# Kernel optimization log

Measured on AMD Instinct MI355X. Metric: run time of the kernel, lower is better.

Reference implementation:

```python
import jax, jax.numpy as jnp
import numpy as np

B, T, D, H = 32, 1024, 1024, 128


def setup_inputs() -> dict:
    key = jax.random.key(0)
    k = jax.random.split(key, 5)
    s = 1.0 / np.sqrt(H)  # pytorch LSTM init scale
    return {
        "x": jax.random.normal(k[0], (B, T, D), dtype=jnp.float32),
        "W_ih": jax.random.uniform(k[1], (4 * H, D), minval=-s, maxval=s, dtype=jnp.float32),
        "W_hh": jax.random.uniform(k[2], (4 * H, H), minval=-s, maxval=s, dtype=jnp.float32),
        "b_ih": jax.random.uniform(k[3], (4 * H,), minval=-s, maxval=s, dtype=jnp.float32),
        "b_hh": jax.random.uniform(k[4], (4 * H,), minval=-s, maxval=s, dtype=jnp.float32),
    }


def reference(x, W_ih, W_hh, b_ih, b_hh):
    # x: [B, T, D]. Single-layer unidirectional LSTM, batch_first, zero init state.
    # Gate order matches PyTorch: i, f, g, o.
    b, t, d = x.shape
    h = W_hh.shape[1]
    # Fuse the input-side GEMM across all timesteps: [B, T, 4H]
    gx = jnp.einsum('btd,gd->btg', x, W_ih) + b_ih + b_hh

    def step(carry, g_t):
        h_prev, c_prev = carry
        g = g_t + h_prev @ W_hh.T  # [B, 4H]
        i, f, gg, o = jnp.split(g, 4, axis=-1)
        i = jax.nn.sigmoid(i)
        f = jax.nn.sigmoid(f)
        gg = jnp.tanh(gg)
        o = jax.nn.sigmoid(o)
        c = f * c_prev + i * gg
        hn = o * jnp.tanh(c)
        return (hn, c), hn

    h0 = jnp.zeros((b, h), dtype=x.dtype)
    c0 = jnp.zeros((b, h), dtype=x.dtype)
    (h_n, c_n), hs = jax.lax.scan(step, (h0, c0), jnp.swapaxes(gx, 0, 1))
    out = jnp.swapaxes(hs, 0, 1)  # [B, T, H]
    # Mirrors torch: (output, (h_n[1,B,H], c_n[1,B,H]))
    return out, h_n[None], c_n[None]
```

## Files before the change

kernel.cpp:

```cpp
#include <hip/hip_runtime.h>
#include <hip/hip_fp16.h>
#include <cstdint>
#include <cstddef>


typedef __attribute__((ext_vector_type(8))) _Float16 half8;
typedef __attribute__((ext_vector_type(4))) _Float16 half4;
typedef __attribute__((ext_vector_type(4))) float    f32x4;

#define BT    32768
#define DD    1024
#define GG    512
#define HH    128
#define TT    1024
#define BB    32

__global__ void prep_kernel(const float* __restrict__ wih,
                            const float* __restrict__ whh,
                            const float* __restrict__ bih,
                            const float* __restrict__ bhh,
                            _Float16* __restrict__ wih_h,
                            __half*   __restrict__ whh_h,
                            float* __restrict__ bsum) {
    int i = blockIdx.x * 256 + threadIdx.x;
    wih_h[i] = (_Float16)wih[i];
    if (i < GG * HH) whh_h[i] = __float2half(whh[i]);
    if (i < GG)      bsum[i] = bih[i] + bhh[i];
}

#define BM 128
#define BN 128
#define BK 32
#define LDP 40

__global__ __launch_bounds__(256)
void gemm_gx(const float* __restrict__ x, const _Float16* __restrict__ wih_h,
             const float* __restrict__ bsum, float* __restrict__ gx) {
    const int bid = blockIdx.x;
    const int m0 = (bid >> 2) * BM;
    const int n0 = (bid & 3) * BN;
    const int t  = threadIdx.x;
    const int lane = t & 63;
    const int w  = t >> 6;
    const int wr = w >> 1, wc = w & 1;
    const int lr = lane & 15;
    const int lk = lane >> 4;

    __shared__ __align__(16) _Float16 As[BM][LDP];
    __shared__ __align__(16) _Float16 Bs[BN][LDP];

    f32x4 acc[4][4] = {};

    for (int kt = 0; kt < DD; kt += BK) {
        #pragma unroll
        for (int pass = 0; pass < 4; ++pass) {
            int r = pass * 32 + (t >> 3);
            int c = (t & 7) * 4;
            float4 v = *(const float4*)(x + (size_t)(m0 + r) * DD + kt + c);
            half4 hv;
            hv[0] = (_Float16)v.x; hv[1] = (_Float16)v.y;
            hv[2] = (_Float16)v.z; hv[3] = (_Float16)v.w;
            *(half4*)&As[r][c] = hv;
        }
        #pragma unroll
        for (int pass = 0; pass < 2; ++pass) {
            int r = pass * 64 + (t >> 2);
            int c = (t & 3) * 8;
            float4 v = *(const float4*)(wih_h + (size_t)(n0 + r) * DD + kt + c);
            *(float4*)&Bs[r][c] = v;
        }
        __syncthreads();

        half8 af[4], bf[4];
        #pragma unroll
        for (int i = 0; i < 4; ++i)
            af[i] = *(const half8*)&As[wr * 64 + i * 16 + lr][lk * 8];
        #pragma unroll
        for (int j = 0; j < 4; ++j)
            bf[j] = *(const half8*)&Bs[wc * 64 + j * 16 + lr][lk * 8];

        #pragma unroll
        for (int i = 0; i < 4; ++i)
            #pragma unroll
            for (int j = 0; j < 4; ++j)
                acc[i][j] = __builtin_amdgcn_mfma_f32_16x16x32_f16(af[i], bf[j], acc[i][j], 0, 0, 0);
        __syncthreads();
    }

    #pragma unroll
    for (int j = 0; j < 4; ++j) {
        int n = n0 + wc * 64 + j * 16 + lr;
        float bn = bsum[n];
        #pragma unroll
        for (int i = 0; i < 4; ++i) {
            int mbase = m0 + wr * 64 + i * 16 + lk * 4;
            #pragma unroll
            for (int r = 0; r < 4; ++r)
                gx[(size_t)(mbase + r) * GG + n] = acc[i][j][r] + bn;
        }
    }
}


__device__ __forceinline__ __half2 u2h(uint32_t v) { return *(__half2*)&v; }

template <int CTRL>
__device__ __forceinline__ float dpp_qp(float x) {
    int i = __float_as_int(x);
    i = __builtin_amdgcn_update_dpp(0, i, CTRL, 0xF, 0xF, true);
    return __int_as_float(i);
}
#define QP_XOR1 0xB1
#define QP_XOR2 0x4E

#define LOG2E   1.4426950408889634f

#define WDECL(Q)  uint32_t w##Q##x, w##Q##y, w##Q##z, w##Q##w;
#define WLOAD(Q)  { uint4 u_ = wp[Q]; w##Q##x = u_.x; w##Q##y = u_.y; \
                    w##Q##z = u_.z; w##Q##w = u_.w; }
#define WPIN(Q)   asm volatile("" : "+v"(w##Q##x), "+v"(w##Q##y), \
                                    "+v"(w##Q##z), "+v"(w##Q##w));
#define DOTE(Q)   { uint4 hv_ = hp[Q]; \
    a0 = __hfma2(u2h(w##Q##x), u2h(hv_.x), a0); \
    a1 = __hfma2(u2h(w##Q##y), u2h(hv_.y), a1); \
    a2 = __hfma2(u2h(w##Q##z), u2h(hv_.z), a2); \
    a3 = __hfma2(u2h(w##Q##w), u2h(hv_.w), a3); }
#define DOTO(Q)   { uint4 hv_ = hp[Q]; \
    a4 = __hfma2(u2h(w##Q##x), u2h(hv_.x), a4); \
    a5 = __hfma2(u2h(w##Q##y), u2h(hv_.y), a5); \
    a6 = __hfma2(u2h(w##Q##z), u2h(hv_.z), a6); \
    a7 = __hfma2(u2h(w##Q##w), u2h(hv_.w), a7); }
#define W16(F) F(0) F(1) F(2) F(3) F(4) F(5) F(6) F(7) \
               F(8) F(9) F(10) F(11) F(12) F(13) F(14) F(15)

__global__ __launch_bounds__(512)
__attribute__((amdgpu_waves_per_eu(2, 2)))
void lstm_rec(const float* __restrict__ gx, const __half* __restrict__ whh_h,
              float* __restrict__ out, float* __restrict__ hn, float* __restrict__ cn) {
    const int b  = blockIdx.x;
    const int t  = threadIdx.x;
    const int j  = t >> 2;
    const int gi = t & 3;
    const int r  = gi * HH + j;

    __shared__ __align__(16) __half hbuf[2][HH];
    __shared__ __align__(16) float  oring[64][HH];

    const uint4* wp = (const uint4*)(whh_h + (size_t)r * HH);
    W16(WDECL)
    W16(WLOAD)
    W16(WPIN)

    const float kneg = (gi == 2) ? -2.f * LOG2E : -LOG2E;
    const float k2   = (gi == 2) ?  2.f : 1.f;
    const float k3   = (gi == 2) ? -1.f : 0.f;

    if (t < HH) hbuf[0][t] = __float2half(0.f);
    __syncthreads();

    const float* gxp  = gx + (size_t)b * TT * GG + r;
    float*       outp = out + (size_t)b * TT * HH;

    float c = 0.f, hval = 0.f;
    float p0 = gxp[0];
    float p1 = gxp[GG];

    for (int step = 0; step < TT; ++step) {
        int sp = step + 2; if (sp > TT - 1) sp = TT - 1;
        float p2 = gxp[(size_t)sp * GG];

        const uint4* hp = (const uint4*)hbuf[step & 1];
        __half2 a0, a1, a2, a3, a4, a5, a6, a7;
        a0 = a1 = a2 = a3 = a4 = a5 = a6 = a7 = __float2half2_rn(0.f);
        DOTE(0)  DOTO(1)  DOTE(2)  DOTO(3)
        DOTE(4)  DOTO(5)  DOTE(6)  DOTO(7)
        DOTE(8)  DOTO(9)  DOTE(10) DOTO(11)
        DOTE(12) DOTO(13) DOTE(14) DOTO(15)
        a0 = __hadd2(a0, a4); a1 = __hadd2(a1, a5);
        a2 = __hadd2(a2, a6); a3 = __hadd2(a3, a7);
        a0 = __hadd2(a0, a2); a1 = __hadd2(a1, a3);
        a0 = __hadd2(a0, a1);
        float pre = p0 + __low2float(a0) + __high2float(a0);

        float s = __builtin_amdgcn_rcpf(1.f + __builtin_amdgcn_exp2f(pre * kneg));
        float a = fmaf(k2, s, k3);

        float x1 = dpp_qp<QP_XOR1>(a);
        float x2 = dpp_qp<QP_XOR2>(a);
        float x3 = dpp_qp<QP_XOR2>(x1);

        if (gi == 0) {
            c = fmaf(x1, c, a * x2);
            float th = fmaf(2.f, __builtin_amdgcn_rcpf(
                          1.f + __builtin_amdgcn_exp2f(-2.f * LOG2E * c)), -1.f);
            hval = x3 * th;
            hbuf[(step + 1) & 1][j] = __float2half(hval);
            oring[step & 63][j] = hval;
        }

        __builtin_amdgcn_sched_barrier(0);
        asm volatile("s_waitcnt lgkmcnt(0)" ::: "memory");
        __builtin_amdgcn_s_barrier();
        __builtin_amdgcn_sched_barrier(0);

        if ((step & 63) == 63) {
            float4*       dst = (float4*)(outp + (size_t)(step - 63) * HH);
            const float4* src = (const float4*)&oring[0][0];
            #pragma unroll
            for (int k = 0; k < 4; ++k)
                dst[t + k * 512] = src[t + k * 512];
            __syncthreads();
        }

        p0 = p1; p1 = p2;
    }

    if (gi == 0) {
        hn[b * HH + j] = hval;
        cn[b * HH + j] = c;
    }
}

extern "C" void kernel_launch(void* const* d_in, const int* in_sizes, int n_in,
                              void* d_out, int out_size, void* d_ws, size_t ws_size,
                              hipStream_t stream) {
    const float* x   = (const float*)d_in[0];
    const float* wih = (const float*)d_in[1];
    const float* whh = (const float*)d_in[2];
    const float* bih = (const float*)d_in[3];
    const float* bhh = (const float*)d_in[4];
    float* out = (float*)d_out;

    char* ws = (char*)d_ws;
    _Float16* wih_h = (_Float16*)ws;
    __half*   whh_h = (__half*)(ws + (size_t)(1 << 20));
    float*    bsum  = (float*)(ws + (size_t)(1 << 20) + (128 << 10));
    float*    gx    = (float*)(ws + (size_t)(1 << 20) + (128 << 10) + 4096);

    prep_kernel<<<(GG * DD) / 256, 256, 0, stream>>>(wih, whh, bih, bhh, wih_h, whh_h, bsum);
    gemm_gx<<<(BT / BM) * (GG / BN), 256, 0, stream>>>(x, wih_h, bsum, gx);

    float* hn = out + (size_t)BB * TT * HH;
    float* cn = hn + BB * HH;
    lstm_rec<<<BB, 512, 0, stream>>>(gx, whh_h, out, hn, cn);
}
```

Measured before the change: 804.1 us.

## Split recurrent dot products along K across quad lanes instead of by gate

Each quad of threads now handles one hidden unit. Each lane covers a quarter of the K dimension for all four gates, and the partial sums are reduced with DPP quad shuffles. Each thread reads only 64 bytes of h from LDS per step instead of 256, which cuts LDS traffic on the serial critical path. In exchange, every lane redundantly evaluates all four gate activations and the cell update, and each lane makes four short FMA chains instead of one long one.

Result: no change. 810.2 us (+0.8%).

```diff
diff --git a/kernel.cpp b/kernel.cpp
--- a/kernel.cpp
+++ b/kernel.cpp
@@ -101,7 +101,6 @@
     }
 }
 
-
 __device__ __forceinline__ __half2 u2h(uint32_t v) { return *(__half2*)&v; }
 
 template <int CTRL>
@@ -115,23 +114,35 @@
 
 #define LOG2E   1.4426950408889634f
 
-#define WDECL(Q)  uint32_t w##Q##x, w##Q##y, w##Q##z, w##Q##w;
-#define WLOAD(Q)  { uint4 u_ = wp[Q]; w##Q##x = u_.x; w##Q##y = u_.y; \
-                    w##Q##z = u_.z; w##Q##w = u_.w; }
-#define WPIN(Q)   asm volatile("" : "+v"(w##Q##x), "+v"(w##Q##y), \
-                                    "+v"(w##Q##z), "+v"(w##Q##w));
-#define DOTE(Q)   { uint4 hv_ = hp[Q]; \
-    a0 = __hfma2(u2h(w##Q##x), u2h(hv_.x), a0); \
-    a1 = __hfma2(u2h(w##Q##y), u2h(hv_.y), a1); \
-    a2 = __hfma2(u2h(w##Q##z), u2h(hv_.z), a2); \
-    a3 = __hfma2(u2h(w##Q##w), u2h(hv_.w), a3); }
-#define DOTO(Q)   { uint4 hv_ = hp[Q]; \
-    a4 = __hfma2(u2h(w##Q##x), u2h(hv_.x), a4); \
-    a5 = __hfma2(u2h(w##Q##y), u2h(hv_.y), a5); \
-    a6 = __hfma2(u2h(w##Q##z), u2h(hv_.z), a6); \
-    a7 = __hfma2(u2h(w##Q##w), u2h(hv_.w), a7); }
-#define W16(F) F(0) F(1) F(2) F(3) F(4) F(5) F(6) F(7) \
-               F(8) F(9) F(10) F(11) F(12) F(13) F(14) F(15)
+#define WDECL(G,Q)  uint32_t w##G##Q##x, w##G##Q##y, w##G##Q##z, w##G##Q##w;
+#define WLOAD(G,Q)  { uint4 u_ = wq[((G) * HH + j) * 16 + 4 * s_ + (Q)]; \
+                      w##G##Q##x = u_.x; w##G##Q##y = u_.y; \
+                      w##G##Q##z = u_.z; w##G##Q##w = u_.w; }
+#define WPIN(G,Q)   asm volatile("" : "+v"(w##G##Q##x), "+v"(w##G##Q##y), \
+                                      "+v"(w##G##Q##z), "+v"(w##G##Q##w));
+#define WALL(F) F(0,0) F(0,1) F(0,2) F(0,3)  F(1,0) F(1,1) F(1,2) F(1,3) \
+                F(2,0) F(2,1) F(2,2) F(2,3)  F(3,0) F(3,1) F(3,2) F(3,3)
+
+#define GATE_DOT(G) {                                          \
+    __half2 cA_ = __float2half2_rn(0.f), cB_ = cA_;            \
+    cA_ = __hfma2(u2h(w##G##0x), u2h(h0.x), cA_);              \
+    cA_ = __hfma2(u2h(w##G##0y), u2h(h0.y), cA_);              \
+    cA_ = __hfma2(u2h(w##G##0z), u2h(h0.z), cA_);              \
+    cA_ = __hfma2(u2h(w##G##0w), u2h(h0.w), cA_);              \
+    cA_ = __hfma2(u2h(w##G##1x), u2h(h1.x), cA_);              \
+    cA_ = __hfma2(u2h(w##G##1y), u2h(h1.y), cA_);              \
+    cA_ = __hfma2(u2h(w##G##1z), u2h(h1.z), cA_);              \
+    cA_ = __hfma2(u2h(w##G##1w), u2h(h1.w), cA_);              \
+    cB_ = __hfma2(u2h(w##G##2x), u2h(h2.x), cB_);              \
+    cB_ = __hfma2(u2h(w##G##2y), u2h(h2.y), cB_);              \
+    cB_ = __hfma2(u2h(w##G##2z), u2h(h2.z), cB_);              \
+    cB_ = __hfma2(u2h(w##G##2w), u2h(h2.w), cB_);              \
+    cB_ = __hfma2(u2h(w##G##3x), u2h(h3.x), cB_);              \
+    cB_ = __hfma2(u2h(w##G##3y), u2h(h3.y), cB_);              \
+    cB_ = __hfma2(u2h(w##G##3z), u2h(h3.z), cB_);              \
+    cB_ = __hfma2(u2h(w##G##3w), u2h(h3.w), cB_);              \
+    __half2 t_ = __hadd2(cA_, cB_);                            \
+    P##G = fmaf(msk##G, p0, __low2float(t_) + __high2float(t_)); }
 
 __global__ __launch_bounds__(512)
 __attribute__((amdgpu_waves_per_eu(2, 2)))
@@ -140,25 +151,25 @@
     const int b  = blockIdx.x;
     const int t  = threadIdx.x;
     const int j  = t >> 2;
-    const int gi = t & 3;
-    const int r  = gi * HH + j;
+    const int s_ = t & 3;
 
     __shared__ __align__(16) __half hbuf[2][HH];
     __shared__ __align__(16) float  oring[64][HH];
 
-    const uint4* wp = (const uint4*)(whh_h + (size_t)r * HH);
-    W16(WDECL)
-    W16(WLOAD)
-    W16(WPIN)
-
-    const float kneg = (gi == 2) ? -2.f * LOG2E : -LOG2E;
-    const float k2   = (gi == 2) ?  2.f : 1.f;
-    const float k3   = (gi == 2) ? -1.f : 0.f;
+    const uint4* wq = (const uint4*)whh_h;
+    WALL(WDECL)
+    WALL(WLOAD)
+    WALL(WPIN)
+
+    const float msk0 = (s_ == 0) ? 1.f : 0.f;
+    const float msk1 = (s_ == 1) ? 1.f : 0.f;
+    const float msk2 = (s_ == 2) ? 1.f : 0.f;
+    const float msk3 = (s_ == 3) ? 1.f : 0.f;
 
     if (t < HH) hbuf[0][t] = __float2half(0.f);
     __syncthreads();
 
-    const float* gxp  = gx + (size_t)b * TT * GG + r;
+    const float* gxp  = gx + (size_t)b * TT * GG + (s_ * HH + j);
     float*       outp = out + (size_t)b * TT * HH;
 
     float c = 0.f, hval = 0.f;
@@ -169,31 +180,30 @@
         int sp = step + 2; if (sp > TT - 1) sp = TT - 1;
         float p2 = gxp[(size_t)sp * GG];
 
-        const uint4* hp = (const uint4*)hbuf[step & 1];
-        __half2 a0, a1, a2, a3, a4, a5, a6, a7;
-        a0 = a1 = a2 = a3 = a4 = a5 = a6 = a7 = __float2half2_rn(0.f);
-        DOTE(0)  DOTO(1)  DOTE(2)  DOTO(3)
-        DOTE(4)  DOTO(5)  DOTE(6)  DOTO(7)
-        DOTE(8)  DOTO(9)  DOTE(10) DOTO(11)
-        DOTE(12) DOTO(13) DOTE(14) DOTO(15)
-        a0 = __hadd2(a0, a4); a1 = __hadd2(a1, a5);
-        a2 = __hadd2(a2, a6); a3 = __hadd2(a3, a7);
-        a0 = __hadd2(a0, a2); a1 = __hadd2(a1, a3);
-        a0 = __hadd2(a0, a1);
-        float pre = p0 + __low2float(a0) + __high2float(a0);
-
-        float s = __builtin_amdgcn_rcpf(1.f + __builtin_amdgcn_exp2f(pre * kneg));
-        float a = fmaf(k2, s, k3);
-
-        float x1 = dpp_qp<QP_XOR1>(a);
-        float x2 = dpp_qp<QP_XOR2>(a);
-        float x3 = dpp_qp<QP_XOR2>(x1);
-
-        if (gi == 0) {
-            c = fmaf(x1, c, a * x2);
-            float th = fmaf(2.f, __builtin_amdgcn_rcpf(
-                          1.f + __builtin_amdgcn_exp2f(-2.f * LOG2E * c)), -1.f);
-            hval = x3 * th;
+        const uint4* hp = (const uint4*)((const char*)hbuf +
+                                         ((step & 1) << 8) + (s_ << 6));
+        uint4 h0 = hp[0], h1 = hp[1], h2 = hp[2], h3 = hp[3];
+
+        float P0, P1, P2, P3;
+        GATE_DOT(0) GATE_DOT(1) GATE_DOT(2) GATE_DOT(3)
+
+        P0 += dpp_qp<QP_XOR1>(P0);  P0 += dpp_qp<QP_XOR2>(P0);
+        P1 += dpp_qp<QP_XOR1>(P1);  P1 += dpp_qp<QP_XOR2>(P1);
+        P2 += dpp_qp<QP_XOR1>(P2);  P2 += dpp_qp<QP_XOR2>(P2);
+        P3 += dpp_qp<QP_XOR1>(P3);  P3 += dpp_qp<QP_XOR2>(P3);
+
+        float A0 = __builtin_amdgcn_rcpf(1.f + __builtin_amdgcn_exp2f(-LOG2E * P0));
+        float A1 = __builtin_amdgcn_rcpf(1.f + __builtin_amdgcn_exp2f(-LOG2E * P1));
+        float A2 = fmaf(2.f, __builtin_amdgcn_rcpf(
+                        1.f + __builtin_amdgcn_exp2f(-2.f * LOG2E * P2)), -1.f);
+        float A3 = __builtin_amdgcn_rcpf(1.f + __builtin_amdgcn_exp2f(-LOG2E * P3));
+
+        c = fmaf(A1, c, A0 * A2);
+        float th = fmaf(2.f, __builtin_amdgcn_rcpf(
+                        1.f + __builtin_amdgcn_exp2f(-2.f * LOG2E * c)), -1.f);
+        hval = A3 * th;
+
+        if (s_ == 0) {
             hbuf[(step + 1) & 1][j] = __float2half(hval);
             oring[step & 63][j] = hval;
         }
@@ -215,7 +225,7 @@
         p0 = p1; p1 = p2;
     }
 
-    if (gi == 0) {
+    if (s_ == 0) {
         hn[b * HH + j] = hval;
         cn[b * HH + j] = c;
     }
```
